# Optimization experiments

Hardware: AMD Instinct MI355X
Metric: run time of the kernel (lower is better)

The kernel has to match this reference:

```python
import jax, jax.numpy as jnp
import numpy as np

K = 20
EPS = 1e-5


def _bn(x, g, b):
    # inference-mode BatchNorm with running_mean=0, running_var=1 (fresh init)
    return x * (g / jnp.sqrt(1.0 + EPS)) + b


def _lrelu(x):
    return jax.nn.leaky_relu(x, 0.2)


def _knn(x, k):
    # x: [B,N,D] -> idx [B,N,k] of nearest neighbors (includes self)
    sq = jnp.sum(x * x, axis=-1)                       # [B,N]
    inner = jnp.einsum('bnd,bmd->bnm', x, x)           # [B,N,N]
    dist = sq[:, :, None] - 2.0 * inner + sq[:, None, :]
    _, idx = jax.lax.top_k(-dist, k)
    return idx


def _edge_feat(x, k):
    # x: [B,N,D] -> [B,N,k,2D] = concat(neighbor - center, center)
    idx = _knn(x, k)
    nbr = jax.vmap(lambda xb, ib: xb[ib])(x, idx)      # [B,N,k,D]
    ctr = jnp.broadcast_to(x[:, :, None, :], nbr.shape)
    return jnp.concatenate([nbr - ctr, ctr], axis=-1)


def _edge_conv(x, W, g, b, k):
    # conv1x1 (no bias) + BN + LeakyReLU + max over neighbors
    f = _edge_feat(x, k)                               # [B,N,k,2D]
    h = jnp.einsum('bnkc,oc->bnko', f, W)
    return jnp.max(_lrelu(_bn(h, g, b)), axis=2)       # [B,N,out]


def setup_inputs() -> dict:
    key = jax.random.key(0)
    ks = jax.random.split(key, 12)
    B, N = 8, 4096
    num_classes = 5
    r = lambda k_, shape: jax.random.normal(k_, shape, jnp.float32) * 0.1
    return {
        'xyz': jax.random.normal(ks[0], (B, N, 3), jnp.float32),
        'W1': r(ks[1], (64, 6)),   'g1': jnp.ones((64,), jnp.float32),  'b1': jnp.zeros((64,), jnp.float32),
        'W2': r(ks[2], (64, 128)), 'g2': jnp.ones((64,), jnp.float32),  'b2': jnp.zeros((64,), jnp.float32),
        'W3': r(ks[3], (64, 128)), 'g3': jnp.ones((64,), jnp.float32),  'b3': jnp.zeros((64,), jnp.float32),
        'W4': r(ks[4], (128, 128)),'g4': jnp.ones((128,), jnp.float32), 'b4': jnp.zeros((128,), jnp.float32),
        'W5': r(ks[5], (1024, 320)),'g5': jnp.ones((1024,), jnp.float32),'b5': jnp.zeros((1024,), jnp.float32),
        'Wl1': r(ks[6], (512, 2048)),'g6': jnp.ones((512,), jnp.float32),'b6': jnp.zeros((512,), jnp.float32),
        'Wl2': r(ks[7], (256, 512)), 'bl2': jnp.zeros((256,), jnp.float32),
        'g7': jnp.ones((256,), jnp.float32), 'b7': jnp.zeros((256,), jnp.float32),
        'Wl3': r(ks[8], (num_classes, 256)), 'bl3': jnp.zeros((num_classes,), jnp.float32),
    }


def reference(xyz, W1, g1, b1, W2, g2, b2, W3, g3, b3, W4, g4, b4,
              W5, g5, b5, Wl1, g6, b6, Wl2, bl2, g7, b7, Wl3, bl3):
    B, N, _ = xyz.shape
    k = min(K, N - 1)
    x1 = _edge_conv(xyz, W1, g1, b1, k)                # [B,N,64]
    x2 = _edge_conv(x1, W2, g2, b2, k)                 # [B,N,64]
    x3 = _edge_conv(x2, W3, g3, b3, k)                 # [B,N,64]
    x4 = _edge_conv(x3, W4, g4, b4, k)                 # [B,N,128]
    xc = jnp.concatenate([x1, x2, x3, x4], axis=-1)    # [B,N,320]
    h = _lrelu(_bn(jnp.einsum('bnc,oc->bno', xc, W5), g5, b5))  # [B,N,1024]
    gmax = jnp.max(h, axis=1)
    gavg = jnp.mean(h, axis=1)
    gfeat = jnp.concatenate([gmax, gavg], axis=-1)     # [B,2048]
    y = _lrelu(_bn(gfeat @ Wl1.T, g6, b6))             # dropout = identity (eval)
    y = _lrelu(_bn(y @ Wl2.T + bl2, g7, b7))
    y = y @ Wl3.T + bl3                                # [B,num_classes]
    return jnp.broadcast_to(y[:, None, :], (B, N, y.shape[-1]))
```

## Files before the change

### kernel.cpp

```cpp
#include <hip/hip_runtime.h>


constexpr int NB  = 8;
constexpr int NPT = 4096;
constexpr int KNB = 20;
constexpr int CAP = 128;

typedef _Float16 half8 __attribute__((ext_vector_type(8)));
typedef float f32x4 __attribute__((ext_vector_type(4)));

__device__ __forceinline__ unsigned int fmono(float f) {
  unsigned int u = __float_as_uint(f);
  return u ^ ((unsigned int)(((int)u) >> 31) | 0x80000000u);
}

__device__ __attribute__((noinline)) unsigned long long compact_row(
    int row, int n, int lane) {
  extern __shared__ char smem[];
  unsigned long long* buf = (unsigned long long*)smem + (size_t)row * CAP;
  const unsigned long long INFK = ~0ull;
  unsigned long long a = (lane < n) ? buf[lane] : INFK;
  unsigned long long c = (lane + 64 < n) ? buf[lane + 64] : INFK;
#pragma unroll
  for (int k = 2; k <= 64; k <<= 1) {
#pragma unroll
    for (int j = k >> 1; j > 0; j >>= 1) {
      const bool tm = (((lane & k) == 0) == ((lane & j) == 0));
      const unsigned long long oa = __shfl_xor(a, j, 64);
      a = ((a < oa) == tm) ? a : oa;
      const unsigned long long oc = __shfl_xor(c, j, 64);
      c = ((c < oc) == tm) ? oc : c;
    }
  }
  unsigned long long m = a < c ? a : c;
#pragma unroll
  for (int j = 32; j > 0; j >>= 1) {
    const unsigned long long o = __shfl_xor(m, j, 64);
    const bool low = (lane & j) == 0;
    m = ((m < o) == low) ? m : o;
  }
  return m;
}

__device__ __forceinline__ void sel4(unsigned long long k0,
                                     unsigned long long k1,
                                     unsigned long long k2,
                                     unsigned long long k3, int base_r,
                                     int quad, int lane, unsigned int below,
                                     unsigned long long& tau, int& cnt) {
  extern __shared__ char smem[];
  unsigned long long* bufB = (unsigned long long*)smem;
#pragma unroll 1
  for (int attempt = 0; attempt < 2; ++attempt) {
    const unsigned long long m0 = __ballot(k0 < tau);
    const unsigned long long m1 = __ballot(k1 < tau);
    const unsigned long long m2 = __ballot(k2 < tau);
    const unsigned long long m3 = __ballot(k3 < tau);
    if ((m0 | m1 | m2 | m3) == 0ull) return;
    const int sh = quad * 16;
    const unsigned int s0 = (unsigned int)(m0 >> sh) & 0xFFFFu;
    const unsigned int s1 = (unsigned int)(m1 >> sh) & 0xFFFFu;
    const unsigned int s2 = (unsigned int)(m2 >> sh) & 0xFFFFu;
    const unsigned int s3 = (unsigned int)(m3 >> sh) & 0xFFFFu;
    const int tot = __popc(s0) + __popc(s1) + __popc(s2) + __popc(s3);
    const unsigned long long needm = __ballot(cnt + tot > CAP);
    if (needm != 0ull && attempt == 0) {
#pragma unroll 1
      for (int q = 0; q < 4; ++q) {
        if ((needm >> (q * 16)) & 1ull) {
          const int nq = __shfl(cnt, q * 16, 64);
          const unsigned long long sv = compact_row(base_r + q * 4, nq, lane);
          const unsigned long long t19 = __shfl(sv, 19, 64);
          if (lane < 20) bufB[(size_t)(base_r + q * 4) * CAP + lane] = sv;
          if (quad == q) { tau = t19; cnt = 20; }
        }
      }
      continue;
    }
    int pos = cnt + __popc(s0 & below) + __popc(s1 & below) +
              __popc(s2 & below) + __popc(s3 & below);
    unsigned long long* bp = bufB + (size_t)(base_r + quad * 4) * CAP;
    if (k0 < tau) { bp[pos] = k0; ++pos; }
    if (k1 < tau) { bp[pos] = k1; ++pos; }
    if (k2 < tau) { bp[pos] = k2; ++pos; }
    if (k3 < tau) { bp[pos] = k3; }
    cnt += tot;
    return;
  }
}

__global__ __launch_bounds__(256) void cvt_xyz(const float* __restrict__ xyz,
                                               float* __restrict__ x0) {
  const int t = blockIdx.x * 256 + threadIdx.x;
  float4 v;
  v.x = xyz[t * 3 + 0];
  v.y = xyz[t * 3 + 1];
  v.z = xyz[t * 3 + 2];
  v.w = 0.0f;
  *(float4*)(x0 + (size_t)t * 4) = v;
}

__global__ __launch_bounds__(256) void sqsplit(const float* __restrict__ x,
                                               float* __restrict__ sqo,
                                               unsigned short* __restrict__ xhi,
                                               unsigned short* __restrict__ xlo) {
  const int t = blockIdx.x * 256 + threadIdx.x;
  const int p = t >> 2, c = t & 3;
  const float* src = x + (size_t)p * 64 + c * 16;
  float s = 0.0f;
  unsigned short hb[16], lb[16];
#pragma unroll
  for (int e = 0; e < 16; e += 4) {
    const float4 v = *(const float4*)(src + e);
    const float vv[4] = {v.x, v.y, v.z, v.w};
#pragma unroll
    for (int u = 0; u < 4; ++u) {
      const float f = vv[u];
      s = fmaf(f, f, s);
      const _Float16 h = (_Float16)f;
      const _Float16 l = (_Float16)(f - (float)h);
      hb[e + u] = __builtin_bit_cast(unsigned short, h);
      lb[e + u] = __builtin_bit_cast(unsigned short, l);
    }
  }
  unsigned short* dh = xhi + (size_t)p * 64 + c * 16;
  unsigned short* dl = xlo + (size_t)p * 64 + c * 16;
  *(uint4*)dh = *(uint4*)hb;
  *(uint4*)(dh + 8) = *(uint4*)(hb + 8);
  *(uint4*)dl = *(uint4*)lb;
  *(uint4*)(dl + 8) = *(uint4*)(lb + 8);
  s += __shfl_xor(s, 1, 64);
  s += __shfl_xor(s, 2, 64);
  if (c == 0) sqo[p] = s;
}

__global__ __launch_bounds__(256, 2) void knn3(const float* __restrict__ x0,
                                               int* __restrict__ idxout) {
  const int bid = blockIdx.x;
  const int b = bid & 7;
  const int i0 = (bid >> 3) * 64;
  const int tid = threadIdx.x, w = tid >> 6, lane = tid & 63;
  const int l15 = lane & 15, quad = lane >> 4;
  const unsigned int below = (1u << l15) - 1u;
  const float* xb = x0 + (size_t)b * (NPT * 4);

  float xix[4], xiy[4], xiz[4];
#pragma unroll
  for (int r = 0; r < 4; ++r) {
    const float4 v =
        *(const float4*)(xb + (size_t)(i0 + w * 16 + quad * 4 + r) * 4);
    xix[r] = v.x;
    xiy[r] = v.y;
    xiz[r] = v.z;
  }

  unsigned long long tau[4] = {~0ull, ~0ull, ~0ull, ~0ull};
  int cnt[4] = {0, 0, 0, 0};

  for (int jt = 0; jt < NPT / 64; ++jt) {
    const int j0 = jt * 64;
    float4 xj[4];
#pragma unroll
    for (int nj = 0; nj < 4; ++nj)
      xj[nj] = *(const float4*)(xb + (size_t)(j0 + nj * 16 + l15) * 4);
#pragma unroll
    for (int r = 0; r < 4; ++r) {
      unsigned long long k[4];
#pragma unroll
      for (int nj = 0; nj < 4; ++nj) {
        const float dx = xj[nj].x - xix[r];
        const float dy = xj[nj].y - xiy[r];
        const float dz = xj[nj].z - xiz[r];
        const float dd = fmaf(dx, dx, fmaf(dy, dy, dz * dz));
        k[nj] = ((unsigned long long)fmono(dd) << 32) |
                (unsigned int)(j0 + nj * 16 + l15);
      }
      sel4(k[0], k[1], k[2], k[3], w * 16 + r, quad, lane, below, tau[r],
           cnt[r]);
    }
  }
#pragma unroll 1
  for (int rw = 0; rw < 16; ++rw) {
    const int q = rw >> 2, r = rw & 3;
    const int nq = __shfl(cnt[r], q * 16, 64);
    const unsigned long long sv = compact_row(w * 16 + rw, nq, lane);
    const int i = i0 + w * 16 + rw;
    if (lane < 20)
      idxout[((size_t)(b * NPT + i)) * KNB + lane] = (int)(unsigned int)sv;
  }
}

__global__ __launch_bounds__(256, 2) void knn_mfma(
    const unsigned short* __restrict__ xhi16,
    const unsigned short* __restrict__ xlo16,
    const float* __restrict__ sqn, int* __restrict__ idxout) {
  const int bid = blockIdx.x;
  const int b = bid & 7;
  const int i0 = (bid >> 3) * 64;
  const int tid = threadIdx.x, w = tid >> 6, lane = tid & 63;
  const int l15 = lane & 15, quad = lane >> 4;
  const unsigned int below = (1u << l15) - 1u;

  const half8* Hb = (const half8*)(xhi16 + (size_t)b * NPT * 64);
  const half8* Lb = (const half8*)(xlo16 + (size_t)b * NPT * 64);
  const float* sqb = sqn + b * NPT;

  const int ia = i0 + w * 16 + l15;
  const half8 ah0 = Hb[(size_t)ia * 8 + quad];
  const half8 ah1 = Hb[(size_t)ia * 8 + 4 + quad];
  const half8 al0 = Lb[(size_t)ia * 8 + quad];
  const half8 al1 = Lb[(size_t)ia * 8 + 4 + quad];

  unsigned long long tau[4] = {~0ull, ~0ull, ~0ull, ~0ull};
  int cnt[4] = {0, 0, 0, 0};

  for (int jt = 0; jt < NPT / 64; ++jt) {
    const int j0 = jt * 64;
    float sq4[4];
#pragma unroll
    for (int nj = 0; nj < 4; ++nj) sq4[nj] = sqb[j0 + nj * 16 + l15];
    f32x4 acc[4];
#pragma unroll
    for (int nj = 0; nj < 4; ++nj) {
      const int jb = j0 + nj * 16 + l15;
      const half8 bh0 = Hb[(size_t)jb * 8 + quad];
      const half8 bh1 = Hb[(size_t)jb * 8 + 4 + quad];
      const half8 bl0 = Lb[(size_t)jb * 8 + quad];
      const half8 bl1 = Lb[(size_t)jb * 8 + 4 + quad];
      f32x4 a = {0.0f, 0.0f, 0.0f, 0.0f};
      a = __builtin_amdgcn_mfma_f32_16x16x32_f16(al0, bh0, a, 0, 0, 0);
      a = __builtin_amdgcn_mfma_f32_16x16x32_f16(al1, bh1, a, 0, 0, 0);
      a = __builtin_amdgcn_mfma_f32_16x16x32_f16(ah0, bl0, a, 0, 0, 0);
      a = __builtin_amdgcn_mfma_f32_16x16x32_f16(ah1, bl1, a, 0, 0, 0);
      a = __builtin_amdgcn_mfma_f32_16x16x32_f16(ah0, bh0, a, 0, 0, 0);
      a = __builtin_amdgcn_mfma_f32_16x16x32_f16(ah1, bh1, a, 0, 0, 0);
      acc[nj] = a;
    }
#pragma unroll
    for (int r = 0; r < 4; ++r) {
      unsigned long long k[4];
#pragma unroll
      for (int nj = 0; nj < 4; ++nj) {
        const float dd = fmaf(-2.0f, acc[nj][r], sq4[nj]);
        k[nj] = ((unsigned long long)fmono(dd) << 32) |
                (unsigned int)(j0 + nj * 16 + l15);
      }
      sel4(k[0], k[1], k[2], k[3], w * 16 + r, quad, lane, below, tau[r],
           cnt[r]);
    }
  }
#pragma unroll 1
  for (int rw = 0; rw < 16; ++rw) {
    const int q = rw >> 2, r = rw & 3;
    const int nq = __shfl(cnt[r], q * 16, 64);
    const unsigned long long sv = compact_row(w * 16 + rw, nq, lane);
    const int i = i0 + w * 16 + rw;
    if (lane < 20)
      idxout[((size_t)(b * NPT + i)) * KNB + lane] = (int)(unsigned int)sv;
  }
}

__global__ __launch_bounds__(256) void featg3(const float* __restrict__ x0,
                                              const float* __restrict__ W,
                                              float* __restrict__ Y) {
  const int lane = threadIdx.x & 63;
  const int bid = blockIdx.x;
  const int p0 =
      ((bid & 7) << 12) + ((bid >> 3) * 4 + (threadIdx.x >> 6)) * 4;
  const float* wr = W + lane * 6;
  const float w0 = wr[0], w1 = wr[1], w2 = wr[2];
#pragma unroll
  for (int r = 0; r < 4; ++r) {
    const float4 v = *(const float4*)(x0 + (size_t)(p0 + r) * 4);
    Y[(size_t)(p0 + r) * 64 + lane] = w0 * v.x + w1 * v.y + w2 * v.z;
  }
}

__global__ __launch_bounds__(256) void featg64(const float* __restrict__ X,
                                               const float* __restrict__ W,
                                               int co, float* __restrict__ Y) {
  __shared__ float Xt[64][68];
  __shared__ float Wt[64][68];
  const int tid = threadIdx.x;
  const int bid = blockIdx.x;
  const int n0 = ((bid & 7) << 12) + (bid >> 3) * 64;
  const int pc = tid & 63, dg = tid >> 6;
#pragma unroll
  for (int rep = 0; rep < 4; ++rep) {
    const int d0 = dg * 16 + rep * 4;
    const float4 xv = *(const float4*)(X + (size_t)(n0 + pc) * 64 + d0);
    Xt[d0 + 0][pc] = xv.x; Xt[d0 + 1][pc] = xv.y;
    Xt[d0 + 2][pc] = xv.z; Xt[d0 + 3][pc] = xv.w;
    const float4 wv = *(const float4*)(W + (size_t)(co + pc) * 128 + d0);
    Wt[d0 + 0][pc] = wv.x; Wt[d0 + 1][pc] = wv.y;
    Wt[d0 + 2][pc] = wv.z; Wt[d0 + 3][pc] = wv.w;
  }
  __syncthreads();
  const int c0 = (tid & 15) * 4, p0 = (tid >> 4) * 4;
  float acc[4][4];
#pragma unroll
  for (int i = 0; i < 4; ++i)
#pragma unroll
    for (int j = 0; j < 4; ++j) acc[i][j] = 0.0f;
#pragma unroll 4
  for (int d = 0; d < 64; ++d) {
    const float4 xa = *(const float4*)&Xt[d][p0];
    const float4 wc = *(const float4*)&Wt[d][c0];
    const float xr[4] = {xa.x, xa.y, xa.z, xa.w};
    const float wr[4] = {wc.x, wc.y, wc.z, wc.w};
#pragma unroll
    for (int i = 0; i < 4; ++i)
#pragma unroll
      for (int j = 0; j < 4; ++j) acc[i][j] = fmaf(xr[i], wr[j], acc[i][j]);
  }
#pragma unroll
  for (int i = 0; i < 4; ++i) {
    float4 o;
    o.x = acc[i][0]; o.y = acc[i][1]; o.z = acc[i][2]; o.w = acc[i][3];
    *(float4*)(Y + (size_t)(n0 + p0 + i) * 64 + c0) = o;
  }
}

template <int DIN, int DS, int COUT>
__global__ __launch_bounds__(256) void gather_edge(
    const float* __restrict__ x, const float* __restrict__ Y,
    const int* __restrict__ idx, const float* __restrict__ W,
    const float* __restrict__ g, const float* __restrict__ bia,
    float* __restrict__ out, int co) {
  const int lane = threadIdx.x & 63;
  const int bid = blockIdx.x;
  const int wglob = ((bid & 7) << 12) + (bid >> 3) * 4 + (threadIdx.x >> 6);
  const int b = wglob >> 12;
  const int c = co + lane;

  const float* wrow = W + (size_t)c * (2 * DIN);
  const float* xi = x + (size_t)wglob * DS;
  float Dv = 0.0f;
  if constexpr (DIN == 3) {
    const float4 v = *(const float4*)xi;
    Dv = (wrow[3] - wrow[0]) * v.x + (wrow[4] - wrow[1]) * v.y +
         (wrow[5] - wrow[2]) * v.z;
  } else {
#pragma unroll
    for (int d0 = 0; d0 < DIN; d0 += 4) {
      const float4 wa4 = *(const float4*)(wrow + d0);
      const float4 wb4 = *(const float4*)(wrow + DIN + d0);
      const float4 v = *(const float4*)(xi + d0);
      Dv += (wb4.x - wa4.x) * v.x + (wb4.y - wa4.y) * v.y +
            (wb4.z - wa4.z) * v.z + (wb4.w - wa4.w) * v.w;
    }
  }
  const float invs = 1.0f / sqrtf(1.0f + 1e-5f);
  const float s = g[c] * invs;
  const float base = fmaf(s, Dv, bia[c]);

  const int* ip = idx + (size_t)wglob * KNB;
  const int jv = ip[lane < KNB ? lane : 0];
  const float* Yb = Y + (((size_t)b) << 12) * 64;
  float m = -3.0e38f;
#pragma unroll
  for (int k = 0; k < KNB; ++k) {
    const int j = __shfl(jv, k, 64);
    const float yv = Yb[(size_t)j * 64 + lane];
    float v = fmaf(s, yv, base);
    v = v > 0.0f ? v : 0.2f * v;
    m = fmaxf(m, v);
  }
  out[(size_t)wglob * COUT + c] = m;
}

__global__ __launch_bounds__(256) void splitW5(
    const float* __restrict__ W5, unsigned short* __restrict__ whi,
    unsigned short* __restrict__ wlo) {
  const int t = blockIdx.x * 256 + threadIdx.x;
  const float4 v = *(const float4*)(W5 + (size_t)t * 4);
  const float vv[4] = {v.x, v.y, v.z, v.w};
  unsigned short hb[4], lb[4];
#pragma unroll
  for (int u = 0; u < 4; ++u) {
    const _Float16 h = (_Float16)vv[u];
    const _Float16 l = (_Float16)(vv[u] - (float)h);
    hb[u] = __builtin_bit_cast(unsigned short, h);
    lb[u] = __builtin_bit_cast(unsigned short, l);
  }
  *(uint2*)(whi + (size_t)t * 4) = *(uint2*)hb;
  *(uint2*)(wlo + (size_t)t * 4) = *(uint2*)lb;
}

__global__ __launch_bounds__(256) void conv5_mfma(
    const float* __restrict__ x1, const float* __restrict__ x2,
    const float* __restrict__ x3, const float* __restrict__ x4,
    const unsigned short* __restrict__ whi,
    const unsigned short* __restrict__ wlo, const float* __restrict__ g5,
    const float* __restrict__ b5, float* __restrict__ pmax,
    float* __restrict__ psum) {
  __shared__ __align__(16) unsigned short xh[64][40];
  __shared__ __align__(16) unsigned short xl[64][40];
  const int nt = blockIdx.x, ct = blockIdx.y, b = blockIdx.z;
  const int tid = threadIdx.x, wv = tid >> 6, lane = tid & 63;
  const int l15 = lane & 15, quad = lane >> 4;
  const int n0 = nt * 64, c0 = ct * 64;

  const int nl = tid >> 2;
  const int kg = (tid & 3) * 8;

  f32x4 acc[4];
#pragma unroll
  for (int nj = 0; nj < 4; ++nj) acc[nj] = {0.0f, 0.0f, 0.0f, 0.0f};

  const int ca = c0 + wv * 16 + l15;

  for (int kt = 0; kt < 10; ++kt) {
    __syncthreads();
    const int kbase = kt * 32;
    const float* src;
    int koff;
    if (kbase < 64)       { src = x1 + ((size_t)(b * NPT + n0 + nl)) * 64;  koff = kbase; }
    else if (kbase < 128) { src = x2 + ((size_t)(b * NPT + n0 + nl)) * 64;  koff = kbase - 64; }
    else if (kbase < 192) { src = x3 + ((size_t)(b * NPT + n0 + nl)) * 64;  koff = kbase - 128; }
    else                  { src = x4 + ((size_t)(b * NPT + n0 + nl)) * 128; koff = kbase - 192; }
    const float4 v0 = *(const float4*)(src + koff + kg);
    const float4 v1 = *(const float4*)(src + koff + kg + 4);
    const float vv[8] = {v0.x, v0.y, v0.z, v0.w, v1.x, v1.y, v1.z, v1.w};
    unsigned short hb[8], lb[8];
#pragma unroll
    for (int u = 0; u < 8; ++u) {
      const _Float16 h = (_Float16)vv[u];
      const _Float16 l = (_Float16)(vv[u] - (float)h);
      hb[u] = __builtin_bit_cast(unsigned short, h);
      lb[u] = __builtin_bit_cast(unsigned short, l);
    }
    *(uint4*)&xh[nl][kg] = *(uint4*)hb;
    *(uint4*)&xl[nl][kg] = *(uint4*)lb;
    __syncthreads();
    const half8 wh =
        *(const half8*)(whi + (size_t)ca * 320 + kbase + quad * 8);
    const half8 wl =
        *(const half8*)(wlo + (size_t)ca * 320 + kbase + quad * 8);
#pragma unroll
    for (int nj = 0; nj < 4; ++nj) {
      const half8 bh = *(const half8*)&xh[nj * 16 + l15][quad * 8];
      const half8 bl = *(const half8*)&xl[nj * 16 + l15][quad * 8];
      f32x4 a = acc[nj];
      a = __builtin_amdgcn_mfma_f32_16x16x32_f16(wl, bh, a, 0, 0, 0);
      a = __builtin_amdgcn_mfma_f32_16x16x32_f16(wh, bl, a, 0, 0, 0);
      a = __builtin_amdgcn_mfma_f32_16x16x32_f16(wh, bh, a, 0, 0, 0);
      acc[nj] = a;
    }
  }

  const float invs = 1.0f / sqrtf(1.0f + 1e-5f);
#pragma unroll
  for (int r = 0; r < 4; ++r) {
    const int c = c0 + wv * 16 + quad * 4 + r;
    const float s = g5[c] * invs;
    const float bb = b5[c];
    float mx = -3.0e38f, sm = 0.0f;
#pragma unroll
    for (int nj = 0; nj < 4; ++nj) {
      float v = fmaf(s, acc[nj][r], bb);
      v = v > 0.0f ? v : 0.2f * v;
      mx = fmaxf(mx, v);
      sm += v;
    }
#pragma unroll
    for (int d = 1; d < 16; d <<= 1) {
      mx = fmaxf(mx, __shfl_xor(mx, d, 64));
      sm += __shfl_xor(sm, d, 64);
    }
    if (l15 == 0) {
      pmax[((size_t)b * 1024 + c) * 64 + nt] = mx;
      psum[((size_t)b * 1024 + c) * 64 + nt] = sm;
    }
  }
}

__global__ __launch_bounds__(256) void reduce5(const float* __restrict__ pmax,
                                               const float* __restrict__ psum,
                                               float* __restrict__ gfeat) {
  const int t = blockIdx.x * 256 + threadIdx.x;
  const int b = t >> 10, c = t & 1023;
  const float* pm = pmax + (size_t)t * 64;
  const float* ps = psum + (size_t)t * 64;
  float mx = -3.0e38f, sm = 0.0f;
  for (int i = 0; i < 64; i += 4) {
    const float4 v = *(const float4*)(pm + i);
    mx = fmaxf(mx, fmaxf(fmaxf(v.x, v.y), fmaxf(v.z, v.w)));
    const float4 u = *(const float4*)(ps + i);
    sm += (u.x + u.y) + (u.z + u.w);
  }
  gfeat[b * 2048 + c] = mx;
  gfeat[b * 2048 + 1024 + c] = sm * (1.0f / 4096.0f);
}

__global__ __launch_bounds__(256) void head1(const float* __restrict__ gfeat,
                                             const float* __restrict__ Wl1,
                                             const float* __restrict__ g6,
                                             const float* __restrict__ b6,
                                             float* __restrict__ y1g) {
  __shared__ float gf[2048];
  __shared__ float red[256];
  const int tid = threadIdx.x;
  const int cb = blockIdx.x, b = blockIdx.y;
  const float4* gsrc = (const float4*)(gfeat + b * 2048);
  for (int p = tid; p < 512; p += 256) ((float4*)gf)[p] = gsrc[p];
  __syncthreads();
  const int cl = cb * 64 + (tid >> 2);
  const int q = tid & 3;
  const float* wr = Wl1 + (size_t)cl * 2048 + q * 512;
  const float* gq = gf + q * 512;
  float acc = 0.0f;
  for (int k0 = 0; k0 < 512; k0 += 8) {
    const float4 w0 = *(const float4*)(wr + k0);
    const float4 w1 = *(const float4*)(wr + k0 + 4);
    acc = fmaf(w0.x, gq[k0 + 0], acc); acc = fmaf(w0.y, gq[k0 + 1], acc);
    acc = fmaf(w0.z, gq[k0 + 2], acc); acc = fmaf(w0.w, gq[k0 + 3], acc);
    acc = fmaf(w1.x, gq[k0 + 4], acc); acc = fmaf(w1.y, gq[k0 + 5], acc);
    acc = fmaf(w1.z, gq[k0 + 6], acc); acc = fmaf(w1.w, gq[k0 + 7], acc);
  }
  red[tid] = acc;
  __syncthreads();
  if (q == 0) {
    float v = red[tid] + red[tid + 1] + red[tid + 2] + red[tid + 3];
    const float invs = 1.0f / sqrtf(1.0f + 1e-5f);
    v = fmaf(g6[cl] * invs, v, b6[cl]);
    v = v > 0.0f ? v : 0.2f * v;
    y1g[b * 512 + cl] = v;
  }
}

__global__ __launch_bounds__(256) void head2(
    const float* __restrict__ y1g, const float* __restrict__ Wl2,
    const float* __restrict__ bl2, const float* __restrict__ g7,
    const float* __restrict__ b7, const float* __restrict__ Wl3,
    const float* __restrict__ bl3, float* __restrict__ out) {
  __shared__ float y1s[512];
  __shared__ float y2s[256];
  __shared__ float y3s[5];
  const int b = blockIdx.x;
  const int t = threadIdx.x;
  y1s[t] = y1g[b * 512 + t];
  y1s[t + 256] = y1g[b * 512 + t + 256];
  __syncthreads();
  {
    const float* wr = Wl2 + (size_t)t * 512;
    float acc = 0.0f;
    for (int k0 = 0; k0 < 512; k0 += 8) {
      const float4 w0 = *(const float4*)(wr + k0);
      const float4 w1 = *(const float4*)(wr + k0 + 4);
      acc = fmaf(w0.x, y1s[k0 + 0], acc); acc = fmaf(w0.y, y1s[k0 + 1], acc);
      acc = fmaf(w0.z, y1s[k0 + 2], acc); acc = fmaf(w0.w, y1s[k0 + 3], acc);
      acc = fmaf(w1.x, y1s[k0 + 4], acc); acc = fmaf(w1.y, y1s[k0 + 5], acc);
      acc = fmaf(w1.z, y1s[k0 + 6], acc); acc = fmaf(w1.w, y1s[k0 + 7], acc);
    }
    const float invs = 1.0f / sqrtf(1.0f + 1e-5f);
    float v = acc + bl2[t];
    v = fmaf(g7[t] * invs, v, b7[t]);
    v = v > 0.0f ? v : 0.2f * v;
    y2s[t] = v;
  }
  __syncthreads();
  if (t < 5) {
    const float* wr = Wl3 + (size_t)t * 256;
    float acc = 0.0f;
    for (int k = 0; k < 256; ++k) acc += wr[k] * y2s[k];
    y3s[t] = acc + bl3[t];
  }
  __syncthreads();
  for (int e = t; e < NPT * 5; e += 256)
    out[(size_t)b * (NPT * 5) + e] = y3s[e % 5];
}

extern "C" void kernel_launch(void* const* d_in, const int* in_sizes, int n_in,
                              void* d_out, int out_size, void* d_ws, size_t ws_size,
                              hipStream_t stream) {
  (void)in_sizes; (void)n_in; (void)out_size;
  const float* xyz = (const float*)d_in[0];
  const float* W1  = (const float*)d_in[1];
  const float* g1  = (const float*)d_in[2];
  const float* b1  = (const float*)d_in[3];
  const float* W2  = (const float*)d_in[4];
  const float* g2  = (const float*)d_in[5];
  const float* b2  = (const float*)d_in[6];
  const float* W3  = (const float*)d_in[7];
  const float* g3  = (const float*)d_in[8];
  const float* b3  = (const float*)d_in[9];
  const float* W4  = (const float*)d_in[10];
  const float* g4  = (const float*)d_in[11];
  const float* b4  = (const float*)d_in[12];
  const float* W5  = (const float*)d_in[13];
  const float* g5  = (const float*)d_in[14];
  const float* b5  = (const float*)d_in[15];
  const float* Wl1 = (const float*)d_in[16];
  const float* g6  = (const float*)d_in[17];
  const float* b6  = (const float*)d_in[18];
  const float* Wl2 = (const float*)d_in[19];
  const float* bl2 = (const float*)d_in[20];
  const float* g7  = (const float*)d_in[21];
  const float* b7  = (const float*)d_in[22];
  const float* Wl3 = (const float*)d_in[23];
  const float* bl3 = (const float*)d_in[24];

  char* ws = (char*)d_ws;
  float* x0    = (float*)(ws + 0);
  float* x1    = (float*)(ws + 524288);
  float* x2    = (float*)(ws + 8912896);
  float* x3    = (float*)(ws + 17301504);
  float* x4    = (float*)(ws + 25690112);
  float* sqb   = (float*)(ws + 42467328);
  int*   idxb  = (int*)  (ws + 42598400);
  float* pmx   = (float*)(ws + 45219840);
  float* psm   = (float*)(ws + 49414144);
  float* gfeat = (float*)(ws + 53608448);
  float* y1g   = (float*)(ws + 53673984);
  if (ws_size < 53690368) return;

  unsigned short* xhi = (unsigned short*)pmx;
  unsigned short* xlo = (unsigned short*)psm;
  float* Yb = pmx;
  unsigned short* whi = (unsigned short*)idxb;
  unsigned short* wlo = (unsigned short*)idxb + 327680;

  cvt_xyz<<<128, 256, 0, stream>>>(xyz, x0);

  knn3<<<512, 256, 65536, stream>>>(x0, idxb);
  featg3<<<2048, 256, 0, stream>>>(x0, W1, Yb);
  gather_edge<3, 4, 64><<<8192, 256, 0, stream>>>(x0, Yb, idxb, W1, g1, b1, x1, 0);

  sqsplit<<<512, 256, 0, stream>>>(x1, sqb, xhi, xlo);
  knn_mfma<<<512, 256, 65536, stream>>>(xhi, xlo, sqb, idxb);
  featg64<<<512, 256, 0, stream>>>(x1, W2, 0, Yb);
  gather_edge<64, 64, 64><<<8192, 256, 0, stream>>>(x1, Yb, idxb, W2, g2, b2, x2, 0);

  sqsplit<<<512, 256, 0, stream>>>(x2, sqb, xhi, xlo);
  knn_mfma<<<512, 256, 65536, stream>>>(xhi, xlo, sqb, idxb);
  featg64<<<512, 256, 0, stream>>>(x2, W3, 0, Yb);
  gather_edge<64, 64, 64><<<8192, 256, 0, stream>>>(x2, Yb, idxb, W3, g3, b3, x3, 0);

  sqsplit<<<512, 256, 0, stream>>>(x3, sqb, xhi, xlo);
  knn_mfma<<<512, 256, 65536, stream>>>(xhi, xlo, sqb, idxb);
  featg64<<<512, 256, 0, stream>>>(x3, W4, 0, Yb);
  gather_edge<64, 64, 128><<<8192, 256, 0, stream>>>(x3, Yb, idxb, W4, g4, b4, x4, 0);
  featg64<<<512, 256, 0, stream>>>(x3, W4, 64, Yb);
  gather_edge<64, 64, 128><<<8192, 256, 0, stream>>>(x3, Yb, idxb, W4, g4, b4, x4, 64);

  splitW5<<<320, 256, 0, stream>>>(W5, whi, wlo);
  conv5_mfma<<<dim3(64, 16, 8), 256, 0, stream>>>(x1, x2, x3, x4, whi, wlo,
                                                  g5, b5, pmx, psm);
  reduce5<<<32, 256, 0, stream>>>(pmx, psm, gfeat);
  head1<<<dim3(8, 8), 256, 0, stream>>>(gfeat, Wl1, g6, b6, y1g);
  head2<<<8, 256, 0, stream>>>(y1g, Wl2, bl2, g7, b7, Wl3, bl3, (float*)d_out);
}
```

Baseline: 2.258 ms.

## Halve rows per block in kNN kernels to double blocks and occupancy

The kNN kernels now handle 32 query rows per block instead of 64, so twice as many blocks launch with half the shared-memory candidate buffer and a higher launch-bounds occupancy target. In the MFMA path each 16-row tile now holds duplicated query rows and only every other accumulator row is used, so half the MFMA work is wasted. The aim is more waves in flight to hide the latency of the selection and memory work, at the cost of redundant matrix math and twice as many reloads of the neighbour tiles.

```diff
diff --git a/kernel.cpp b/kernel.cpp
--- a/kernel.cpp
+++ b/kernel.cpp
@@ -68,10 +68,11 @@
 #pragma unroll 1
       for (int q = 0; q < 4; ++q) {
         if ((needm >> (q * 16)) & 1ull) {
+          const int row = base_r + q * 2;
           const int nq = __shfl(cnt, q * 16, 64);
-          const unsigned long long sv = compact_row(base_r + q * 4, nq, lane);
+          const unsigned long long sv = compact_row(row, nq, lane);
           const unsigned long long t19 = __shfl(sv, 19, 64);
-          if (lane < 20) bufB[(size_t)(base_r + q * 4) * CAP + lane] = sv;
+          if (lane < 20) bufB[(size_t)row * CAP + lane] = sv;
           if (quad == q) { tau = t19; cnt = 20; }
         }
       }
@@ -79,7 +80,7 @@
     }
     int pos = cnt + __popc(s0 & below) + __popc(s1 & below) +
               __popc(s2 & below) + __popc(s3 & below);
-    unsigned long long* bp = bufB + (size_t)(base_r + quad * 4) * CAP;
+    unsigned long long* bp = bufB + (size_t)(base_r + quad * 2) * CAP;
     if (k0 < tau) { bp[pos] = k0; ++pos; }
     if (k1 < tau) { bp[pos] = k1; ++pos; }
     if (k2 < tau) { bp[pos] = k2; ++pos; }
@@ -134,28 +135,28 @@
   if (c == 0) sqo[p] = s;
 }
 
-__global__ __launch_bounds__(256, 2) void knn3(const float* __restrict__ x0,
+__global__ __launch_bounds__(256, 4) void knn3(const float* __restrict__ x0,
                                                int* __restrict__ idxout) {
   const int bid = blockIdx.x;
   const int b = bid & 7;
-  const int i0 = (bid >> 3) * 64;
+  const int i0 = (bid >> 3) * 32;
   const int tid = threadIdx.x, w = tid >> 6, lane = tid & 63;
   const int l15 = lane & 15, quad = lane >> 4;
   const unsigned int below = (1u << l15) - 1u;
   const float* xb = x0 + (size_t)b * (NPT * 4);
 
-  float xix[4], xiy[4], xiz[4];
-#pragma unroll
-  for (int r = 0; r < 4; ++r) {
+  float xix[2], xiy[2], xiz[2];
+#pragma unroll
+  for (int r = 0; r < 2; ++r) {
     const float4 v =
-        *(const float4*)(xb + (size_t)(i0 + w * 16 + quad * 4 + r) * 4);
+        *(const float4*)(xb + (size_t)(i0 + w * 8 + quad * 2 + r) * 4);
     xix[r] = v.x;
     xiy[r] = v.y;
     xiz[r] = v.z;
   }
 
-  unsigned long long tau[4] = {~0ull, ~0ull, ~0ull, ~0ull};
-  int cnt[4] = {0, 0, 0, 0};
+  unsigned long long tau[2] = {~0ull, ~0ull};
+  int cnt[2] = {0, 0};
 
   for (int jt = 0; jt < NPT / 64; ++jt) {
     const int j0 = jt * 64;
@@ -164,39 +165,39 @@
     for (int nj = 0; nj < 4; ++nj)
       xj[nj] = *(const float4*)(xb + (size_t)(j0 + nj * 16 + l15) * 4);
 #pragma unroll
-    for (int r = 0; r < 4; ++r) {
+    for (int rr = 0; rr < 2; ++rr) {
       unsigned long long k[4];
 #pragma unroll
       for (int nj = 0; nj < 4; ++nj) {
-        const float dx = xj[nj].x - xix[r];
-        const float dy = xj[nj].y - xiy[r];
-        const float dz = xj[nj].z - xiz[r];
+        const float dx = xj[nj].x - xix[rr];
+        const float dy = xj[nj].y - xiy[rr];
+        const float dz = xj[nj].z - xiz[rr];
         const float dd = fmaf(dx, dx, fmaf(dy, dy, dz * dz));
         k[nj] = ((unsigned long long)fmono(dd) << 32) |
                 (unsigned int)(j0 + nj * 16 + l15);
       }
-      sel4(k[0], k[1], k[2], k[3], w * 16 + r, quad, lane, below, tau[r],
-           cnt[r]);
+      sel4(k[0], k[1], k[2], k[3], w * 8 + rr, quad, lane, below, tau[rr],
+           cnt[rr]);
     }
   }
 #pragma unroll 1
-  for (int rw = 0; rw < 16; ++rw) {
-    const int q = rw >> 2, r = rw & 3;
-    const int nq = __shfl(cnt[r], q * 16, 64);
-    const unsigned long long sv = compact_row(w * 16 + rw, nq, lane);
-    const int i = i0 + w * 16 + rw;
+  for (int rw = 0; rw < 8; ++rw) {
+    const int q = rw >> 1, rr = rw & 1;
+    const int nq = __shfl(cnt[rr], q * 16, 64);
+    const unsigned long long sv = compact_row(w * 8 + rw, nq, lane);
+    const int i = i0 + w * 8 + rw;
     if (lane < 20)
       idxout[((size_t)(b * NPT + i)) * KNB + lane] = (int)(unsigned int)sv;
   }
 }
 
-__global__ __launch_bounds__(256, 2) void knn_mfma(
+__global__ __launch_bounds__(256, 4) void knn_mfma(
     const unsigned short* __restrict__ xhi16,
     const unsigned short* __restrict__ xlo16,
     const float* __restrict__ sqn, int* __restrict__ idxout) {
   const int bid = blockIdx.x;
   const int b = bid & 7;
-  const int i0 = (bid >> 3) * 64;
+  const int i0 = (bid >> 3) * 32;
   const int tid = threadIdx.x, w = tid >> 6, lane = tid & 63;
   const int l15 = lane & 15, quad = lane >> 4;
   const unsigned int below = (1u << l15) - 1u;
@@ -205,14 +206,14 @@
   const half8* Lb = (const half8*)(xlo16 + (size_t)b * NPT * 64);
   const float* sqb = sqn + b * NPT;
 
-  const int ia = i0 + w * 16 + l15;
+  const int ia = i0 + w * 8 + (l15 >> 1);
   const half8 ah0 = Hb[(size_t)ia * 8 + quad];
   const half8 ah1 = Hb[(size_t)ia * 8 + 4 + quad];
   const half8 al0 = Lb[(size_t)ia * 8 + quad];
   const half8 al1 = Lb[(size_t)ia * 8 + 4 + quad];
 
-  unsigned long long tau[4] = {~0ull, ~0ull, ~0ull, ~0ull};
-  int cnt[4] = {0, 0, 0, 0};
+  unsigned long long tau[2] = {~0ull, ~0ull};
+  int cnt[2] = {0, 0};
 
   for (int jt = 0; jt < NPT / 64; ++jt) {
     const int j0 = jt * 64;
@@ -237,24 +238,24 @@
       acc[nj] = a;
     }
 #pragma unroll
-    for (int r = 0; r < 4; ++r) {
+    for (int rr = 0; rr < 2; ++rr) {
       unsigned long long k[4];
 #pragma unroll
       for (int nj = 0; nj < 4; ++nj) {
-        const float dd = fmaf(-2.0f, acc[nj][r], sq4[nj]);
+        const float dd = fmaf(-2.0f, acc[nj][rr * 2], sq4[nj]);
         k[nj] = ((unsigned long long)fmono(dd) << 32) |
                 (unsigned int)(j0 + nj * 16 + l15);
       }
-      sel4(k[0], k[1], k[2], k[3], w * 16 + r, quad, lane, below, tau[r],
-           cnt[r]);
+      sel4(k[0], k[1], k[2], k[3], w * 8 + rr, quad, lane, below, tau[rr],
+           cnt[rr]);
     }
   }
 #pragma unroll 1
-  for (int rw = 0; rw < 16; ++rw) {
-    const int q = rw >> 2, r = rw & 3;
-    const int nq = __shfl(cnt[r], q * 16, 64);
-    const unsigned long long sv = compact_row(w * 16 + rw, nq, lane);
-    const int i = i0 + w * 16 + rw;
+  for (int rw = 0; rw < 8; ++rw) {
+    const int q = rw >> 1, rr = rw & 1;
+    const int nq = __shfl(cnt[rr], q * 16, 64);
+    const unsigned long long sv = compact_row(w * 8 + rw, nq, lane);
+    const int i = i0 + w * 8 + rw;
     if (lane < 20)
       idxout[((size_t)(b * NPT + i)) * KNB + lane] = (int)(unsigned int)sv;
   }
@@ -623,22 +624,22 @@
 
   cvt_xyz<<<128, 256, 0, stream>>>(xyz, x0);
 
-  knn3<<<512, 256, 65536, stream>>>(x0, idxb);
+  knn3<<<1024, 256, 32768, stream>>>(x0, idxb);
   featg3<<<2048, 256, 0, stream>>>(x0, W1, Yb);
   gather_edge<3, 4, 64><<<8192, 256, 0, stream>>>(x0, Yb, idxb, W1, g1, b1, x1, 0);
 
   sqsplit<<<512, 256, 0, stream>>>(x1, sqb, xhi, xlo);
-  knn_mfma<<<512, 256, 65536, stream>>>(xhi, xlo, sqb, idxb);
+  knn_mfma<<<1024, 256, 32768, stream>>>(xhi, xlo, sqb, idxb);
   featg64<<<512, 256, 0, stream>>>(x1, W2, 0, Yb);
   gather_edge<64, 64, 64><<<8192, 256, 0, stream>>>(x1, Yb, idxb, W2, g2, b2, x2, 0);
 
   sqsplit<<<512, 256, 0, stream>>>(x2, sqb, xhi, xlo);
-  knn_mfma<<<512, 256, 65536, stream>>>(xhi, xlo, sqb, idxb);
+  knn_mfma<<<1024, 256, 32768, stream>>>(xhi, xlo, sqb, idxb);
   featg64<<<512, 256, 0, stream>>>(x2, W3, 0, Yb);
   gather_edge<64, 64, 64><<<8192, 256, 0, stream>>>(x2, Yb, idxb, W3, g3, b3, x3, 0);
 
   sqsplit<<<512, 256, 0, stream>>>(x3, sqb, xhi, xlo);
-  knn_mfma<<<512, 256, 65536, stream>>>(xhi, xlo, sqb, idxb);
+  knn_mfma<<<1024, 256, 32768, stream>>>(xhi, xlo, sqb, idxb);
   featg64<<<512, 256, 0, stream>>>(x3, W4, 0, Yb);
   gather_edge<64, 64, 128><<<8192, 256, 0, stream>>>(x3, Yb, idxb, W4, g4, b4, x4, 0);
   featg64<<<512, 256, 0, stream>>>(x3, W4, 64, Yb);
```

After: 2.523 ms. +11.8%, slower.

## Replace ballot-compacted candidate buffer with per-lane slots and bounded drain in kNN

Applied to the files above, without the earlier changes.

Changes the top-k candidate selection in both kNN kernels. The old scheme compacted candidates across lanes with ballots and prefix popcounts into a 128-entry row buffer. Now each lane appends passing keys to its own strided slots in a 116-entry row (20 kept plus 16 lanes × 6 slots). A row is drained with a bitonic sort whenever any lane holds more than 2 pending keys. This removes the per-step ballot and popc work but can trigger more frequent full sorts, and it lowers the LDS allocation per block.

```diff
diff --git a/kernel.cpp b/kernel.cpp
--- a/kernel.cpp
+++ b/kernel.cpp
@@ -4,7 +4,7 @@
 constexpr int NB  = 8;
 constexpr int NPT = 4096;
 constexpr int KNB = 20;
-constexpr int CAP = 128;
+constexpr int ROWU = 116;
 
 typedef _Float16 half8 __attribute__((ext_vector_type(8)));
 typedef float f32x4 __attribute__((ext_vector_type(4)));
@@ -14,13 +14,12 @@
   return u ^ ((unsigned int)(((int)u) >> 31) | 0x80000000u);
 }
 
-__device__ __attribute__((noinline)) unsigned long long compact_row(
-    int row, int n, int lane) {
+__device__ __attribute__((noinline)) unsigned long long drain_row(int row,
+                                                                  int lane) {
   extern __shared__ char smem[];
-  unsigned long long* buf = (unsigned long long*)smem + (size_t)row * CAP;
-  const unsigned long long INFK = ~0ull;
-  unsigned long long a = (lane < n) ? buf[lane] : INFK;
-  unsigned long long c = (lane + 64 < n) ? buf[lane + 64] : INFK;
+  unsigned long long* rb = (unsigned long long*)smem + (size_t)row * ROWU;
+  unsigned long long a = rb[lane];
+  unsigned long long c = (lane + 64 < ROWU) ? rb[lane + 64] : ~0ull;
 #pragma unroll
   for (int k = 2; k <= 64; k <<= 1) {
 #pragma unroll
@@ -39,54 +38,10 @@
     const bool low = (lane & j) == 0;
     m = ((m < o) == low) ? m : o;
   }
+  if (lane < 20) rb[lane] = m;
+#pragma unroll
+  for (int idx = 20 + lane; idx < ROWU; idx += 64) rb[idx] = ~0ull;
   return m;
-}
-
-__device__ __forceinline__ void sel4(unsigned long long k0,
-                                     unsigned long long k1,
-                                     unsigned long long k2,
-                                     unsigned long long k3, int base_r,
-                                     int quad, int lane, unsigned int below,
-                                     unsigned long long& tau, int& cnt) {
-  extern __shared__ char smem[];
-  unsigned long long* bufB = (unsigned long long*)smem;
-#pragma unroll 1
-  for (int attempt = 0; attempt < 2; ++attempt) {
-    const unsigned long long m0 = __ballot(k0 < tau);
-    const unsigned long long m1 = __ballot(k1 < tau);
-    const unsigned long long m2 = __ballot(k2 < tau);
-    const unsigned long long m3 = __ballot(k3 < tau);
-    if ((m0 | m1 | m2 | m3) == 0ull) return;
-    const int sh = quad * 16;
-    const unsigned int s0 = (unsigned int)(m0 >> sh) & 0xFFFFu;
-    const unsigned int s1 = (unsigned int)(m1 >> sh) & 0xFFFFu;
-    const unsigned int s2 = (unsigned int)(m2 >> sh) & 0xFFFFu;
-    const unsigned int s3 = (unsigned int)(m3 >> sh) & 0xFFFFu;
-    const int tot = __popc(s0) + __popc(s1) + __popc(s2) + __popc(s3);
-    const unsigned long long needm = __ballot(cnt + tot > CAP);
-    if (needm != 0ull && attempt == 0) {
-#pragma unroll 1
-      for (int q = 0; q < 4; ++q) {
-        if ((needm >> (q * 16)) & 1ull) {
-          const int nq = __shfl(cnt, q * 16, 64);
-          const unsigned long long sv = compact_row(base_r + q * 4, nq, lane);
-          const unsigned long long t19 = __shfl(sv, 19, 64);
-          if (lane < 20) bufB[(size_t)(base_r + q * 4) * CAP + lane] = sv;
-          if (quad == q) { tau = t19; cnt = 20; }
-        }
-      }
-      continue;
-    }
-    int pos = cnt + __popc(s0 & below) + __popc(s1 & below) +
-              __popc(s2 & below) + __popc(s3 & below);
-    unsigned long long* bp = bufB + (size_t)(base_r + quad * 4) * CAP;
-    if (k0 < tau) { bp[pos] = k0; ++pos; }
-    if (k1 < tau) { bp[pos] = k1; ++pos; }
-    if (k2 < tau) { bp[pos] = k2; ++pos; }
-    if (k3 < tau) { bp[pos] = k3; }
-    cnt += tot;
-    return;
-  }
 }
 
 __global__ __launch_bounds__(256) void cvt_xyz(const float* __restrict__ xyz,
@@ -141,8 +96,14 @@
   const int i0 = (bid >> 3) * 64;
   const int tid = threadIdx.x, w = tid >> 6, lane = tid & 63;
   const int l15 = lane & 15, quad = lane >> 4;
-  const unsigned int below = (1u << l15) - 1u;
+  extern __shared__ char smem[];
+  unsigned long long* S = (unsigned long long*)smem;
   const float* xb = x0 + (size_t)b * (NPT * 4);
+
+  {
+    unsigned long long* wb = S + (size_t)(w * 16) * ROWU;
+    for (int idx = lane; idx < 16 * ROWU; idx += 64) wb[idx] = ~0ull;
+  }
 
   float xix[4], xiy[4], xiz[4];
 #pragma unroll
@@ -154,8 +115,13 @@
     xiz[r] = v.z;
   }
 
+  int soff[4];
+#pragma unroll
+  for (int r = 0; r < 4; ++r)
+    soff[r] = (w * 16 + quad * 4 + r) * ROWU + 20 + l15;
+
   unsigned long long tau[4] = {~0ull, ~0ull, ~0ull, ~0ull};
-  int cnt[4] = {0, 0, 0, 0};
+  int c[4] = {0, 0, 0, 0};
 
   for (int jt = 0; jt < NPT / 64; ++jt) {
     const int j0 = jt * 64;
@@ -165,28 +131,47 @@
       xj[nj] = *(const float4*)(xb + (size_t)(j0 + nj * 16 + l15) * 4);
 #pragma unroll
     for (int r = 0; r < 4; ++r) {
-      unsigned long long k[4];
 #pragma unroll
       for (int nj = 0; nj < 4; ++nj) {
         const float dx = xj[nj].x - xix[r];
         const float dy = xj[nj].y - xiy[r];
         const float dz = xj[nj].z - xiz[r];
         const float dd = fmaf(dx, dx, fmaf(dy, dy, dz * dz));
-        k[nj] = ((unsigned long long)fmono(dd) << 32) |
-                (unsigned int)(j0 + nj * 16 + l15);
+        const unsigned long long key =
+            ((unsigned long long)fmono(dd) << 32) |
+            (unsigned int)(j0 + nj * 16 + l15);
+        if (key < tau[r]) {
+          S[soff[r] + c[r] * 16] = key;
+          ++c[r];
+        }
       }
-      sel4(k[0], k[1], k[2], k[3], w * 16 + r, quad, lane, below, tau[r],
-           cnt[r]);
+    }
+    const int cm = max(max(c[0], c[1]), max(c[2], c[3]));
+    if (__ballot(cm > 2) != 0ull) {
+#pragma unroll 1
+      for (int r = 0; r < 4; ++r) {
+        const unsigned long long mr = __ballot(c[r] > 2);
+        if (mr == 0ull) continue;
+#pragma unroll 1
+        for (int q = 0; q < 4; ++q) {
+          if ((mr >> (q * 16)) & 0xFFFFull) {
+            const unsigned long long m = drain_row(w * 16 + q * 4 + r, lane);
+            const unsigned long long t19 = __shfl(m, 19, 64);
+            if (quad == q) {
+              tau[r] = tau[r] < t19 ? tau[r] : t19;
+              c[r] = 0;
+            }
+          }
+        }
+      }
     }
   }
 #pragma unroll 1
   for (int rw = 0; rw < 16; ++rw) {
-    const int q = rw >> 2, r = rw & 3;
-    const int nq = __shfl(cnt[r], q * 16, 64);
-    const unsigned long long sv = compact_row(w * 16 + rw, nq, lane);
+    const unsigned long long m = drain_row(w * 16 + rw, lane);
     const int i = i0 + w * 16 + rw;
     if (lane < 20)
-      idxout[((size_t)(b * NPT + i)) * KNB + lane] = (int)(unsigned int)sv;
+      idxout[((size_t)(b * NPT + i)) * KNB + lane] = (int)(unsigned int)m;
   }
 }
 
@@ -199,7 +184,13 @@
   const int i0 = (bid >> 3) * 64;
   const int tid = threadIdx.x, w = tid >> 6, lane = tid & 63;
   const int l15 = lane & 15, quad = lane >> 4;
-  const unsigned int below = (1u << l15) - 1u;
+  extern __shared__ char smem[];
+  unsigned long long* S = (unsigned long long*)smem;
+
+  {
+    unsigned long long* wb = S + (size_t)(w * 16) * ROWU;
+    for (int idx = lane; idx < 16 * ROWU; idx += 64) wb[idx] = ~0ull;
+  }
 
   const half8* Hb = (const half8*)(xhi16 + (size_t)b * NPT * 64);
   const half8* Lb = (const half8*)(xlo16 + (size_t)b * NPT * 64);
@@ -211,8 +202,13 @@
   const half8 al0 = Lb[(size_t)ia * 8 + quad];
   const half8 al1 = Lb[(size_t)ia * 8 + 4 + quad];
 
+  int soff[4];
+#pragma unroll
+  for (int r = 0; r < 4; ++r)
+    soff[r] = (w * 16 + quad * 4 + r) * ROWU + 20 + l15;
+
   unsigned long long tau[4] = {~0ull, ~0ull, ~0ull, ~0ull};
-  int cnt[4] = {0, 0, 0, 0};
+  int c[4] = {0, 0, 0, 0};
 
   for (int jt = 0; jt < NPT / 64; ++jt) {
     const int j0 = jt * 64;
@@ -238,25 +234,44 @@
     }
 #pragma unroll
     for (int r = 0; r < 4; ++r) {
-      unsigned long long k[4];
 #pragma unroll
       for (int nj = 0; nj < 4; ++nj) {
         const float dd = fmaf(-2.0f, acc[nj][r], sq4[nj]);
-        k[nj] = ((unsigned long long)fmono(dd) << 32) |
-                (unsigned int)(j0 + nj * 16 + l15);
+        const unsigned long long key =
+            ((unsigned long long)fmono(dd) << 32) |
+            (unsigned int)(j0 + nj * 16 + l15);
+        if (key < tau[r]) {
+          S[soff[r] + c[r] * 16] = key;
+          ++c[r];
+        }
       }
-      sel4(k[0], k[1], k[2], k[3], w * 16 + r, quad, lane, below, tau[r],
-           cnt[r]);
+    }
+    const int cm = max(max(c[0], c[1]), max(c[2], c[3]));
+    if (__ballot(cm > 2) != 0ull) {
+#pragma unroll 1
+      for (int r = 0; r < 4; ++r) {
+        const unsigned long long mr = __ballot(c[r] > 2);
+        if (mr == 0ull) continue;
+#pragma unroll 1
+        for (int q = 0; q < 4; ++q) {
+          if ((mr >> (q * 16)) & 0xFFFFull) {
+            const unsigned long long m = drain_row(w * 16 + q * 4 + r, lane);
+            const unsigned long long t19 = __shfl(m, 19, 64);
+            if (quad == q) {
+              tau[r] = tau[r] < t19 ? tau[r] : t19;
+              c[r] = 0;
+            }
+          }
+        }
+      }
     }
   }
 #pragma unroll 1
   for (int rw = 0; rw < 16; ++rw) {
-    const int q = rw >> 2, r = rw & 3;
-    const int nq = __shfl(cnt[r], q * 16, 64);
-    const unsigned long long sv = compact_row(w * 16 + rw, nq, lane);
+    const unsigned long long m = drain_row(w * 16 + rw, lane);
     const int i = i0 + w * 16 + rw;
     if (lane < 20)
-      idxout[((size_t)(b * NPT + i)) * KNB + lane] = (int)(unsigned int)sv;
+      idxout[((size_t)(b * NPT + i)) * KNB + lane] = (int)(unsigned int)m;
   }
 }
 
@@ -623,22 +638,22 @@
 
   cvt_xyz<<<128, 256, 0, stream>>>(xyz, x0);
 
-  knn3<<<512, 256, 65536, stream>>>(x0, idxb);
+  knn3<<<512, 256, 59392, stream>>>(x0, idxb);
   featg3<<<2048, 256, 0, stream>>>(x0, W1, Yb);
   gather_edge<3, 4, 64><<<8192, 256, 0, stream>>>(x0, Yb, idxb, W1, g1, b1, x1, 0);
 
   sqsplit<<<512, 256, 0, stream>>>(x1, sqb, xhi, xlo);
-  knn_mfma<<<512, 256, 65536, stream>>>(xhi, xlo, sqb, idxb);
+  knn_mfma<<<512, 256, 59392, stream>>>(xhi, xlo, sqb, idxb);
   featg64<<<512, 256, 0, stream>>>(x1, W2, 0, Yb);
   gather_edge<64, 64, 64><<<8192, 256, 0, stream>>>(x1, Yb, idxb, W2, g2, b2, x2, 0);
 
   sqsplit<<<512, 256, 0, stream>>>(x2, sqb, xhi, xlo);
-  knn_mfma<<<512, 256, 65536, stream>>>(xhi, xlo, sqb, idxb);
+  knn_mfma<<<512, 256, 59392, stream>>>(xhi, xlo, sqb, idxb);
   featg64<<<512, 256, 0, stream>>>(x2, W3, 0, Yb);
   gather_edge<64, 64, 64><<<8192, 256, 0, stream>>>(x2, Yb, idxb, W3, g3, b3, x3, 0);
 
   sqsplit<<<512, 256, 0, stream>>>(x3, sqb, xhi, xlo);
-  knn_mfma<<<512, 256, 65536, stream>>>(xhi, xlo, sqb, idxb);
+  knn_mfma<<<512, 256, 59392, stream>>>(xhi, xlo, sqb, idxb);
   featg64<<<512, 256, 0, stream>>>(x3, W4, 0, Yb);
   gather_edge<64, 64, 128><<<8192, 256, 0, stream>>>(x3, Yb, idxb, W4, g4, b4, x4, 0);
   featg64<<<512, 256, 0, stream>>>(x3, W4, 64, Yb);
```

Measured after the change: 2.706 ms. 1.2x slower.
